# Performance work log

Measured on AMD Instinct MI355X. Metric: run time of the kernel, lower is better.

Reference implementation:

```python
import jax, jax.numpy as jnp
import numpy as np
from jax import lax

BITS = 8
CLIP = 2.0 ** (BITS - 1) - 1.0  # 127 for int8 symmetric quantization
EPS = 1e-6


def _quantize(x):
    """Dynamic per-tensor symmetric quantization (AQT-style).

    Returns the integer-valued (but float-dtype) quantized tensor and the
    scale such that dequant = q / scale.
    """
    bound = jnp.maximum(jnp.max(jnp.abs(x)), EPS)
    scale = CLIP / bound
    q = jnp.clip(jnp.round(x * scale), -CLIP, CLIP)
    return q, scale


def setup_inputs() -> dict:
    key = jax.random.key(0)
    k1, k2 = jax.random.split(key)
    lhs = jax.random.normal(k1, (4096, 4096), dtype=jnp.float32)
    rhs = jax.random.normal(k2, (4096, 4096), dtype=jnp.float32)
    return {"lhs": lhs, "rhs": rhs}


def reference(lhs, rhs):
    # Quantize both operands with dynamically computed per-tensor scales,
    # do the matmul on the integer-valued tensors, then dequantize the
    # result by the product of scales. This is the math aqt_ops.aqt_dot
    q_lhs, s_lhs = _quantize(lhs)
    q_rhs, s_rhs = _quantize(rhs)
    acc = jnp.matmul(q_lhs, q_rhs)  # [M, N], integer-valued accumulation
    return acc / (s_lhs * s_rhs)
```

## Files before the change

### kernel.cpp

```cpp
#include <hip/hip_runtime.h>
#include <hip/hip_bf16.h>


typedef int v4i __attribute__((ext_vector_type(4)));
typedef int v16i __attribute__((ext_vector_type(16)));

#define MAT_N 4096

__device__ __forceinline__ void async_copy16(const void* g, void* l) {
    __builtin_amdgcn_global_load_lds(
        (const __attribute__((address_space(1))) void*)g,
        (__attribute__((address_space(3))) void*)l,
        16, 0, 0);
}

__device__ __forceinline__ unsigned uabs_bits(float f) {
    return __float_as_uint(f) & 0x7fffffffu;
}

__global__ __launch_bounds__(256) void absmax_partial_kernel(
    const float4* __restrict__ lhs, const float4* __restrict__ rhs,
    unsigned* __restrict__ pmax) {
    const int b = blockIdx.x;
    const float4* x = (b < 512) ? lhs : rhs;
    const float4* p = x + (size_t)(b & 511) * 8192;
    unsigned m0 = 0, m1 = 0, m2 = 0, m3 = 0;
#pragma unroll 8
    for (int u = 0; u < 32; u++) {
        float4 v = p[u * 256 + threadIdx.x];
        m0 = max(m0, uabs_bits(v.x));
        m1 = max(m1, uabs_bits(v.y));
        m2 = max(m2, uabs_bits(v.z));
        m3 = max(m3, uabs_bits(v.w));
    }
    unsigned m = max(max(m0, m1), max(m2, m3));
#pragma unroll
    for (int off = 32; off > 0; off >>= 1)
        m = max(m, (unsigned)__shfl_down(m, off, 64));
    __shared__ unsigned sm[4];
    if ((threadIdx.x & 63) == 0) sm[threadIdx.x >> 6] = m;
    __syncthreads();
    if (threadIdx.x == 0)
        pmax[b] = max(max(sm[0], sm[1]), max(sm[2], sm[3]));
}

__global__ __launch_bounds__(256) void quant_fused_kernel(
    const float* __restrict__ lhs, const float* __restrict__ rhs,
    unsigned char* __restrict__ qA, signed char* __restrict__ qBT,
    const unsigned* __restrict__ pmax) {
    const int N = MAT_N;
    const int t = threadIdx.x;
    int b = blockIdx.x;
    __shared__ __align__(16) signed char smT[64 * 80];
    __shared__ unsigned red[4];
    __shared__ float s_sh;

    const int slot0 = (b < 4096) ? 0 : 512;
    unsigned mm = max(pmax[slot0 + t], pmax[slot0 + 256 + t]);
#pragma unroll
    for (int off = 32; off > 0; off >>= 1)
        mm = max(mm, (unsigned)__shfl_down(mm, off, 64));
    if ((t & 63) == 0) red[t >> 6] = mm;
    __syncthreads();
    if (t == 0) {
        unsigned f = max(max(red[0], red[1]), max(red[2], red[3]));
        s_sh = 127.0f / fmaxf(__uint_as_float(f), 1e-6f);
    }
    __syncthreads();
    const float s = s_sh;

    if (b < 4096) {
        const float4* x4 = (const float4*)lhs;
        unsigned* q4 = (unsigned*)qA;
        const int base4 = b * 1024;
#pragma unroll
        for (int u = 0; u < 4; u++) {
            int idx = base4 + u * 256 + t;
            float4 v = x4[idx];
            int a = min(127, max(-127, (int)rintf(v.x * s)));
            int bq = min(127, max(-127, (int)rintf(v.y * s)));
            int c = min(127, max(-127, (int)rintf(v.z * s)));
            int d = min(127, max(-127, (int)rintf(v.w * s)));
            q4[idx] = (unsigned)(a & 0xff) | ((unsigned)(bq & 0xff) << 8) |
                      ((unsigned)(c & 0xff) << 16) | ((unsigned)(d & 0xff) << 24);
        }
    } else {
        b -= 4096;
        const int n0 = (b & 63) * 64;
        const int k0 = (b >> 6) * 64;
        const int mk = t >> 4;
        const int mn = t & 15;
        const float4* x4 = (const float4*)rhs;

        unsigned w[4];
#pragma unroll
        for (int i = 0; i < 4; i++) {
            float4 v = x4[(size_t)(k0 + 4 * mk + i) * (N / 4) + (n0 >> 2) + mn];
            int a = min(127, max(-127, (int)rintf(v.x * s)));
            int bq = min(127, max(-127, (int)rintf(v.y * s)));
            int c = min(127, max(-127, (int)rintf(v.z * s)));
            int d = min(127, max(-127, (int)rintf(v.w * s)));
            w[i] = (unsigned)(a & 0xff) | ((unsigned)(bq & 0xff) << 8) |
                   ((unsigned)(c & 0xff) << 16) | ((unsigned)(d & 0xff) << 24);
        }
#pragma unroll
        for (int j = 0; j < 4; j++) {
            unsigned selj = (unsigned)j | ((unsigned)(4 + j) << 8) |
                            ((unsigned)j << 16) | ((unsigned)(4 + j) << 24);
            unsigned p01 = __builtin_amdgcn_perm(w[1], w[0], selj);
            unsigned p23 = __builtin_amdgcn_perm(w[3], w[2], selj);
            unsigned uj = __builtin_amdgcn_perm(p23, p01, 0x05040100u);
            *(unsigned*)(smT + (4 * mn + j) * 80 + 4 * mk) = uj;
        }
        __syncthreads();
        const int nr = t >> 2;
        const int kq = (t & 3) * 16;
        int4 val = *(const int4*)(smT + nr * 80 + kq);
        *(int4*)(qBT + (size_t)(n0 + nr) * N + k0 + kq) = val;
    }
}

__global__ __launch_bounds__(512, 2) void gemm_i8_kernel(
    const signed char* __restrict__ A, const signed char* __restrict__ BT,
    float* __restrict__ C, const unsigned* __restrict__ pmax) {
    const int N = MAT_N;
    __shared__ __align__(16) signed char As[2][256 * 128];
    __shared__ __align__(16) signed char Bs[2][256 * 128];
    __shared__ unsigned redl[8], redr[8];

    const int tid = threadIdx.x;
    const int wave = tid >> 6;
    const int lane = tid & 63;
    const int m32 = lane & 31;
    const int h = lane >> 5;
    const int wm = wave >> 2;
    const int wn = wave & 3;

    const int bid = blockIdx.x;
    const int xcd = bid & 7;
    const int bi = bid >> 3;
    const int by = (xcd >> 1) * 4 + (bi >> 3);
    const int bx = (xcd & 1) * 8 + (bi & 7);
    const int brow = by * 256;
    const int bcol = bx * 256;

    v16i acc[4][2] = {};

    int gaoff[4], gboff[4], lofs[4];
#pragma unroll
    for (int u = 0; u < 4; u++) {
        int c = tid + 512 * u;
        int r = c >> 3;
        int q = (c & 7) ^ ((r ^ (r >> 3)) & 7);
        gaoff[u] = (brow + r) * N + q * 16;
        gboff[u] = (bcol + r) * N + q * 16;
        lofs[u] = c * 16;
    }

    int arow[4], av[4];
#pragma unroll
    for (int mi = 0; mi < 4; mi++) {
        int r = wm * 128 + mi * 32 + m32;
        arow[mi] = r * 128;
        av[mi] = (r ^ (r >> 3)) & 7;
    }
    int bro[2], bv[2];
#pragma unroll
    for (int nj = 0; nj < 2; nj++) {
        int r = wn * 64 + nj * 32 + m32;
        bro[nj] = r * 128;
        bv[nj] = (r ^ (r >> 3)) & 7;
    }

    auto stage = [&](int buf, int koff) {
#pragma unroll
        for (int u = 0; u < 4; u++)
            async_copy16(A + gaoff[u] + koff, &As[buf][lofs[u]]);
#pragma unroll
        for (int u = 0; u < 4; u++)
            async_copy16(BT + gboff[u] + koff, &Bs[buf][lofs[u]]);
    };

    auto slice = [&](const signed char* as_, const signed char* bs_, int s) {
        v4i af[4], bf[2];
        const int q = 2 * s + h;
#pragma unroll
        for (int mi = 0; mi < 4; mi++)
            af[mi] = *(const v4i*)(as_ + arow[mi] + ((q ^ av[mi]) << 4));
#pragma unroll
        for (int nj = 0; nj < 2; nj++)
            bf[nj] = *(const v4i*)(bs_ + bro[nj] + ((q ^ bv[nj]) << 4));
        __builtin_amdgcn_s_setprio(1);
#pragma unroll
        for (int mi = 0; mi < 4; mi++)
#pragma unroll
            for (int nj = 0; nj < 2; nj++)
                acc[mi][nj] = __builtin_amdgcn_mfma_i32_32x32x32_i8(
                    af[mi], bf[nj], acc[mi][nj], 0, 0, 0);
        __builtin_amdgcn_s_setprio(0);
    };

    stage(0, 0);
    stage(1, 128);
    asm volatile("s_waitcnt vmcnt(8)" ::: "memory");
    __builtin_amdgcn_s_barrier();
    __builtin_amdgcn_sched_barrier(0);

    for (int t = 0; t < 30; ++t) {
        const signed char* as_ = As[t & 1];
        const signed char* bs_ = Bs[t & 1];
        slice(as_, bs_, 0);
        slice(as_, bs_, 1);
        slice(as_, bs_, 2);
        slice(as_, bs_, 3);
        __builtin_amdgcn_s_barrier();
        __builtin_amdgcn_sched_barrier(0);
        stage(t & 1, (t + 2) * 128);
        asm volatile("s_waitcnt vmcnt(8)" ::: "memory");
        __builtin_amdgcn_s_barrier();
        __builtin_amdgcn_sched_barrier(0);
    }
    {
        const signed char* as_ = As[0];
        const signed char* bs_ = Bs[0];
        slice(as_, bs_, 0);
        slice(as_, bs_, 1);
        slice(as_, bs_, 2);
        slice(as_, bs_, 3);
        asm volatile("s_waitcnt vmcnt(0)" ::: "memory");
        __builtin_amdgcn_s_barrier();
        __builtin_amdgcn_sched_barrier(0);
    }
    {
        const signed char* as_ = As[1];
        const signed char* bs_ = Bs[1];
        slice(as_, bs_, 0);
        slice(as_, bs_, 1);
        slice(as_, bs_, 2);
        slice(as_, bs_, 3);
    }

    unsigned ml = pmax[tid];
    unsigned mr = pmax[512 + tid];
#pragma unroll
    for (int off = 32; off > 0; off >>= 1) {
        ml = max(ml, (unsigned)__shfl_down(ml, off, 64));
        mr = max(mr, (unsigned)__shfl_down(mr, off, 64));
    }
    if (lane == 0) { redl[wave] = ml; redr[wave] = mr; }
    __syncthreads();
    unsigned fl = redl[0], fr = redr[0];
#pragma unroll
    for (int k = 1; k < 8; k++) {
        fl = max(fl, redl[k]);
        fr = max(fr, redr[k]);
    }
    const float bl = fmaxf(__uint_as_float(fl), 1e-6f);
    const float br = fmaxf(__uint_as_float(fr), 1e-6f);
    const float dq = bl * br * (1.0f / (127.0f * 127.0f));

#pragma unroll
    for (int mi = 0; mi < 4; mi++)
#pragma unroll
        for (int nj = 0; nj < 2; nj++) {
            const int col = bcol + wn * 64 + nj * 32 + m32;
#pragma unroll
            for (int reg = 0; reg < 16; reg++) {
                const int row =
                    brow + wm * 128 + mi * 32 + (reg & 3) + 8 * (reg >> 2) + 4 * h;
                C[(size_t)row * N + col] = (float)acc[mi][nj][reg] * dq;
            }
        }
}

extern "C" void kernel_launch(void* const* d_in, const int* in_sizes, int n_in,
                              void* d_out, int out_size, void* d_ws, size_t ws_size,
                              hipStream_t stream) {
    const float* lhs = (const float*)d_in[0];
    const float* rhs = (const float*)d_in[1];
    float* out = (float*)d_out;

    unsigned* pmax = (unsigned*)d_ws;
    signed char* qA = (signed char*)d_ws + 8192;
    signed char* qBT = qA + (size_t)MAT_N * MAT_N;

    absmax_partial_kernel<<<1024, 256, 0, stream>>>(
        (const float4*)lhs, (const float4*)rhs, pmax);
    quant_fused_kernel<<<8192, 256, 0, stream>>>(
        lhs, rhs, (unsigned char*)qA, qBT, pmax);
    gemm_i8_kernel<<<256, 512, 0, stream>>>(qA, qBT, out, pmax);
}
```

Baseline: 256.2 us.

## Restructure GEMM main loop into four-phase ping-pong schedule with split prefetch

Replaces the two-deep prefetch pipeline (stage two tiles ahead, wait with vmcnt(8)) with a one-ahead double buffer. Each K-iteration is split into four phases, each loading LDS fragments and then issuing eight MFMAs, with barriers between phases so the waves interleave memory and compute. The A and B prefetches are issued in separate phases to spread global load traffic. The cost is many more barriers per iteration and a shallower prefetch distance, which may expose global memory latency.

```diff
diff --git a/kernel.cpp b/kernel.cpp
--- a/kernel.cpp
+++ b/kernel.cpp
@@ -120,6 +120,10 @@
     }
 }
 
+#define MFMA_I8 __builtin_amdgcn_mfma_i32_32x32x32_i8
+#define SBAR0() __builtin_amdgcn_sched_barrier(0)
+#define BARRIER() __builtin_amdgcn_s_barrier()
+
 __global__ __launch_bounds__(512, 2) void gemm_i8_kernel(
     const signed char* __restrict__ A, const signed char* __restrict__ BT,
     float* __restrict__ C, const unsigned* __restrict__ pmax) {
@@ -172,72 +176,123 @@
         bv[nj] = (r ^ (r >> 3)) & 7;
     }
 
-    auto stage = [&](int buf, int koff) {
-#pragma unroll
-        for (int u = 0; u < 4; u++)
-            async_copy16(A + gaoff[u] + koff, &As[buf][lofs[u]]);
-#pragma unroll
-        for (int u = 0; u < 4; u++)
-            async_copy16(BT + gboff[u] + koff, &Bs[buf][lofs[u]]);
-    };
-
-    auto slice = [&](const signed char* as_, const signed char* bs_, int s) {
-        v4i af[4], bf[2];
-        const int q = 2 * s + h;
-#pragma unroll
-        for (int mi = 0; mi < 4; mi++)
-            af[mi] = *(const v4i*)(as_ + arow[mi] + ((q ^ av[mi]) << 4));
-#pragma unroll
-        for (int nj = 0; nj < 2; nj++)
-            bf[nj] = *(const v4i*)(bs_ + bro[nj] + ((q ^ bv[nj]) << 4));
-        __builtin_amdgcn_s_setprio(1);
-#pragma unroll
-        for (int mi = 0; mi < 4; mi++)
-#pragma unroll
-            for (int nj = 0; nj < 2; nj++)
-                acc[mi][nj] = __builtin_amdgcn_mfma_i32_32x32x32_i8(
-                    af[mi], bf[nj], acc[mi][nj], 0, 0, 0);
-        __builtin_amdgcn_s_setprio(0);
-    };
-
-    stage(0, 0);
-    stage(1, 128);
-    asm volatile("s_waitcnt vmcnt(8)" ::: "memory");
-    __builtin_amdgcn_s_barrier();
-    __builtin_amdgcn_sched_barrier(0);
-
-    for (int t = 0; t < 30; ++t) {
+#pragma unroll
+    for (int u = 0; u < 4; u++) async_copy16(A + gaoff[u], &As[0][lofs[u]]);
+#pragma unroll
+    for (int u = 0; u < 4; u++) async_copy16(BT + gboff[u], &Bs[0][lofs[u]]);
+    asm volatile("s_waitcnt vmcnt(0)" ::: "memory");
+    BARRIER();
+    SBAR0();
+
+    for (int t = 0; t < 32; ++t) {
         const signed char* as_ = As[t & 1];
         const signed char* bs_ = Bs[t & 1];
-        slice(as_, bs_, 0);
-        slice(as_, bs_, 1);
-        slice(as_, bs_, 2);
-        slice(as_, bs_, 3);
-        __builtin_amdgcn_s_barrier();
-        __builtin_amdgcn_sched_barrier(0);
-        stage(t & 1, (t + 2) * 128);
-        asm volatile("s_waitcnt vmcnt(8)" ::: "memory");
-        __builtin_amdgcn_s_barrier();
-        __builtin_amdgcn_sched_barrier(0);
-    }
-    {
-        const signed char* as_ = As[0];
-        const signed char* bs_ = Bs[0];
-        slice(as_, bs_, 0);
-        slice(as_, bs_, 1);
-        slice(as_, bs_, 2);
-        slice(as_, bs_, 3);
-        asm volatile("s_waitcnt vmcnt(0)" ::: "memory");
-        __builtin_amdgcn_s_barrier();
-        __builtin_amdgcn_sched_barrier(0);
-    }
-    {
-        const signed char* as_ = As[1];
-        const signed char* bs_ = Bs[1];
-        slice(as_, bs_, 0);
-        slice(as_, bs_, 1);
-        slice(as_, bs_, 2);
-        slice(as_, bs_, 3);
+        signed char* na = As[(t & 1) ^ 1];
+        signed char* nb = Bs[(t & 1) ^ 1];
+        const int nko = (t + 1) * 128;
+        const bool st = (t < 31);
+
+#define LDA_(mi, s) (*(const v4i*)(as_ + arow[mi] + (((2 * (s) + h) ^ av[mi]) << 4)))
+#define LDB_(nj, s) (*(const v4i*)(bs_ + bro[nj] + (((2 * (s) + h) ^ bv[nj]) << 4)))
+
+        v4i bf00, bf01, bf10, bf11;
+
+        {
+            v4i a00 = LDA_(0, 0), a01 = LDA_(0, 1);
+            v4i a10 = LDA_(1, 0), a11 = LDA_(1, 1);
+            bf00 = LDB_(0, 0); bf01 = LDB_(0, 1);
+            bf10 = LDB_(1, 0); bf11 = LDB_(1, 1);
+            if (st) {
+#pragma unroll
+                for (int u = 0; u < 4; u++)
+                    async_copy16(A + gaoff[u] + nko, na + lofs[u]);
+            }
+            SBAR0();
+            BARRIER();
+            asm volatile("s_waitcnt lgkmcnt(0)" ::: "memory");
+            SBAR0();
+            __builtin_amdgcn_s_setprio(1);
+            acc[0][0] = MFMA_I8(a00, bf00, acc[0][0], 0, 0, 0);
+            acc[0][1] = MFMA_I8(a00, bf10, acc[0][1], 0, 0, 0);
+            acc[1][0] = MFMA_I8(a10, bf00, acc[1][0], 0, 0, 0);
+            acc[1][1] = MFMA_I8(a10, bf10, acc[1][1], 0, 0, 0);
+            acc[0][0] = MFMA_I8(a01, bf01, acc[0][0], 0, 0, 0);
+            acc[0][1] = MFMA_I8(a01, bf11, acc[0][1], 0, 0, 0);
+            acc[1][0] = MFMA_I8(a11, bf01, acc[1][0], 0, 0, 0);
+            acc[1][1] = MFMA_I8(a11, bf11, acc[1][1], 0, 0, 0);
+            __builtin_amdgcn_s_setprio(0);
+            BARRIER();
+        }
+        {
+            v4i a20 = LDA_(2, 0), a21 = LDA_(2, 1);
+            v4i a30 = LDA_(3, 0), a31 = LDA_(3, 1);
+            if (st) {
+#pragma unroll
+                for (int u = 0; u < 4; u++)
+                    async_copy16(BT + gboff[u] + nko, nb + lofs[u]);
+            }
+            SBAR0();
+            BARRIER();
+            asm volatile("s_waitcnt lgkmcnt(0)" ::: "memory");
+            SBAR0();
+            __builtin_amdgcn_s_setprio(1);
+            acc[2][0] = MFMA_I8(a20, bf00, acc[2][0], 0, 0, 0);
+            acc[2][1] = MFMA_I8(a20, bf10, acc[2][1], 0, 0, 0);
+            acc[3][0] = MFMA_I8(a30, bf00, acc[3][0], 0, 0, 0);
+            acc[3][1] = MFMA_I8(a30, bf10, acc[3][1], 0, 0, 0);
+            acc[2][0] = MFMA_I8(a21, bf01, acc[2][0], 0, 0, 0);
+            acc[2][1] = MFMA_I8(a21, bf11, acc[2][1], 0, 0, 0);
+            acc[3][0] = MFMA_I8(a31, bf01, acc[3][0], 0, 0, 0);
+            acc[3][1] = MFMA_I8(a31, bf11, acc[3][1], 0, 0, 0);
+            __builtin_amdgcn_s_setprio(0);
+            BARRIER();
+        }
+        {
+            v4i a00 = LDA_(0, 2), a01 = LDA_(0, 3);
+            v4i a10 = LDA_(1, 2), a11 = LDA_(1, 3);
+            bf00 = LDB_(0, 2); bf01 = LDB_(0, 3);
+            bf10 = LDB_(1, 2); bf11 = LDB_(1, 3);
+            SBAR0();
+            BARRIER();
+            asm volatile("s_waitcnt lgkmcnt(0)" ::: "memory");
+            SBAR0();
+            __builtin_amdgcn_s_setprio(1);
+            acc[0][0] = MFMA_I8(a00, bf00, acc[0][0], 0, 0, 0);
+            acc[0][1] = MFMA_I8(a00, bf10, acc[0][1], 0, 0, 0);
+            acc[1][0] = MFMA_I8(a10, bf00, acc[1][0], 0, 0, 0);
+            acc[1][1] = MFMA_I8(a10, bf10, acc[1][1], 0, 0, 0);
+            acc[0][0] = MFMA_I8(a01, bf01, acc[0][0], 0, 0, 0);
+            acc[0][1] = MFMA_I8(a01, bf11, acc[0][1], 0, 0, 0);
+            acc[1][0] = MFMA_I8(a11, bf01, acc[1][0], 0, 0, 0);
+            acc[1][1] = MFMA_I8(a11, bf11, acc[1][1], 0, 0, 0);
+            __builtin_amdgcn_s_setprio(0);
+            BARRIER();
+        }
+        {
+            v4i a20 = LDA_(2, 2), a21 = LDA_(2, 3);
+            v4i a30 = LDA_(3, 2), a31 = LDA_(3, 3);
+            SBAR0();
+            BARRIER();
+            asm volatile("s_waitcnt lgkmcnt(0)" ::: "memory");
+            SBAR0();
+            __builtin_amdgcn_s_setprio(1);
+            acc[2][0] = MFMA_I8(a20, bf00, acc[2][0], 0, 0, 0);
+            acc[2][1] = MFMA_I8(a20, bf10, acc[2][1], 0, 0, 0);
+            acc[3][0] = MFMA_I8(a30, bf00, acc[3][0], 0, 0, 0);
+            acc[3][1] = MFMA_I8(a30, bf10, acc[3][1], 0, 0, 0);
+            acc[2][0] = MFMA_I8(a21, bf01, acc[2][0], 0, 0, 0);
+            acc[2][1] = MFMA_I8(a21, bf11, acc[2][1], 0, 0, 0);
+            acc[3][0] = MFMA_I8(a31, bf01, acc[3][0], 0, 0, 0);
+            acc[3][1] = MFMA_I8(a31, bf11, acc[3][1], 0, 0, 0);
+            __builtin_amdgcn_s_setprio(0);
+            if (st) {
+                asm volatile("s_waitcnt vmcnt(0)" ::: "memory");
+            }
+            BARRIER();
+            SBAR0();
+        }
+#undef LDA_
+#undef LDB_
     }
 
     unsigned ml = pmax[tid];
```

New measurement: 264.8 us. +3.4%, slower.
